# Performance work log

Measured on AMD Instinct MI355X. Metric: run time of the kernel, lower is better.

The kernel has to match this reference:

```python
import jax, jax.numpy as jnp
import numpy as np

N, E, FN, FE, H, B = 8192, 32768, 32, 16, 73, 64
T_MP, T_S2S = 3, 12


def setup_inputs() -> dict:
    key = jax.random.key(0)
    k = jax.random.split(key, 24)
    s = 0.1
    p = lambda i, shape: jax.random.normal(k[i], shape, jnp.float32) * s
    return {
        "node_feats": jax.random.normal(k[0], (N, FN), jnp.float32),
        "edge_feats": jax.random.normal(k[1], (E, FE), jnp.float32),
        "W_in": p(2, (FN, H)), "b_in": p(3, (H,)),
        "ee_W1": p(4, (FE, H)), "ee_b1": p(5, (H,)),
        "ee_W2": p(6, (H, H * H)), "ee_b2": p(7, (H * H,)),
        "gru_Wih": p(8, (3 * H, H)), "gru_Whh": p(9, (3 * H, H)),
        "gru_bih": p(10, (3 * H,)), "gru_bhh": p(11, (3 * H,)),
        "lstm_Wih": p(12, (4 * H, 2 * H)), "lstm_Whh": p(13, (4 * H, H)),
        "lstm_bih": p(14, (4 * H,)), "lstm_bhh": p(15, (4 * H,)),
        "W_out": p(16, (H, 1)), "b_out": p(17, (1,)),
        "Esrc": jax.random.randint(k[18], (E,), 0, N),
        "Etgt": jax.random.randint(k[19], (E,), 0, N),
        "batch": jnp.sort(jax.random.randint(k[20], (N,), 0, B)),
    }


def reference(node_feats, edge_feats, W_in, b_in, ee_W1, ee_b1, ee_W2, ee_b2,
              gru_Wih, gru_Whh, gru_bih, gru_bhh,
              lstm_Wih, lstm_Whh, lstm_bih, lstm_bhh, W_out, b_out,
              Esrc, Etgt, batch):
    # EdgeEncoderMLP: edge features -> per-edge HxH weight matrices (Gilmer edge network)
    A = (jax.nn.relu(edge_feats @ ee_W1 + ee_b1) @ ee_W2 + ee_b2).reshape(E, H, H)
    h = node_feats @ W_in + b_in  # [N, H]

    def mp_step(h, _):
        m = jnp.einsum('eij,ej->ei', A, h[Esrc])           # per-edge matvec (gather-matmul)
        agg = jax.ops.segment_sum(m, Etgt, num_segments=N)  # scatter-add to targets
        # GRUCell update (torch gate order r,z,n)
        gi = agg @ gru_Wih.T + gru_bih
        gh = h @ gru_Whh.T + gru_bhh
        ir, iz, inn = jnp.split(gi, 3, axis=-1)
        hr, hz, hn = jnp.split(gh, 3, axis=-1)
        r = jax.nn.sigmoid(ir + hr)
        z = jax.nn.sigmoid(iz + hz)
        n = jnp.tanh(inn + r * hn)
        return (1.0 - z) * n + z * h, None

    h, _ = jax.lax.scan(mp_step, h, None, length=T_MP)

    # Set2Set pooling with a 1-layer LSTM (torch gate order i,f,g,o)
    def s2s_step(carry, _):
        q_star, hh, cc = carry
        gates = q_star @ lstm_Wih.T + lstm_bih + hh @ lstm_Whh.T + lstm_bhh
        i, f, g, o = jnp.split(gates, 4, axis=-1)
        cc = jax.nn.sigmoid(f) * cc + jax.nn.sigmoid(i) * jnp.tanh(g)
        hh = jax.nn.sigmoid(o) * jnp.tanh(cc)
        q = hh                                              # [B, H]
        e = jnp.sum(h * q[batch], axis=-1)                  # [N] attention logits
        emax = jax.ops.segment_max(e, batch, num_segments=B)
        a = jnp.exp(e - emax[batch])
        a = a / jax.ops.segment_sum(a, batch, num_segments=B)[batch]
        r = jax.ops.segment_sum(a[:, None] * h, batch, num_segments=B)
        return (jnp.concatenate([q, r], axis=-1), hh, cc), None

    init = (jnp.zeros((B, 2 * H), h.dtype), jnp.zeros((B, H), h.dtype),
            jnp.zeros((B, H), h.dtype))
    (q_star, _, _), _ = jax.lax.scan(s2s_step, init, None, length=T_S2S)
    return q_star[:, :H] @ W_out + b_out  # [B, 1]
```

## Files before the change

### kernel.cpp

```cpp
#include <hip/hip_runtime.h>

typedef _Float16 f16;
typedef f16 f16x2 __attribute__((ext_vector_type(2)));
typedef f16 f16x4 __attribute__((ext_vector_type(4)));
typedef f16 f16x8 __attribute__((ext_vector_type(8)));
typedef float f32x4 __attribute__((ext_vector_type(4)));

#define AS1 __attribute__((address_space(1)))
#define AS3 __attribute__((address_space(3)))

#define NN 8192
#define EE 32768

#if __has_builtin(__builtin_amdgcn_fdot2)
#define HAS_FDOT2 1
#else
#define HAS_FDOT2 0
#endif

__device__ __forceinline__ void glds16(const void* g, void* l) {
  __builtin_amdgcn_global_load_lds((const AS1 unsigned int*)g, (AS3 unsigned int*)l, 16, 0, 0);
}
__device__ __forceinline__ void stage_bytes(const void* g, void* s, int nbytes, int tid) {
  const int lane = tid & 63;
  for (int off = tid * 16; off < nbytes; off += 4096)
    glds16((const char*)g + off, (char*)s + (off - lane * 16));
}

__global__ void prep_kernel(
    const float* __restrict__ nf, const float* __restrict__ ef,
    const float* __restrict__ W_in, const float* __restrict__ b_in,
    const float* __restrict__ W1, const float* __restrict__ b1,
    const float* __restrict__ W2, const float* __restrict__ b2,
    const float* __restrict__ gWih, const float* __restrict__ gWhh,
    const float* __restrict__ lWih, const float* __restrict__ lWhh,
    const int* __restrict__ batch, const int* __restrict__ Etgt,
    float* __restrict__ h, f16* __restrict__ hf, f16* __restrict__ ehh,
    f16* __restrict__ W2f, f16* __restrict__ WihT, f16* __restrict__ WhhT,
    f16* __restrict__ Wcat, int* __restrict__ segstarts,
    int* __restrict__ count, int* __restrict__ bucket) {
  int t = blockIdx.x * 256 + threadIdx.x;
  if (t < 786432) {
    int n = t / 96, i = t - n * 96;
    float v = 0.f;
    if (i < 73) {
      v = b_in[i];
      const float* nr = nf + n * 32;
      #pragma unroll
      for (int f = 0; f < 32; ++f) v += nr[f] * W_in[f * 73 + i];
    }
    h[t] = v; hf[t] = (f16)v;
    return;
  }
  t -= 786432;
  if (t < 2621440) {
    int e = t / 80, k = t - e * 80;
    float v;
    if (k < 73) {
      v = b1[k];
      const float* er = ef + e * 16;
      #pragma unroll
      for (int f = 0; f < 16; ++f) v += er[f] * W1[f * 73 + k];
      v = fmaxf(v, 0.f);
    } else v = (k == 73) ? 1.f : 0.f;
    ehh[t] = (f16)v;
    return;
  }
  t -= 2621440;
  if (t < 614400) {
    int kg = t / 7680, r = t - kg * 7680;
    int nt = r / 1536, r2 = r - nt * 1536;
    int ks = r2 / 512, r3 = r2 - ks * 512;
    int l = r3 >> 3, j = r3 & 7;
    int mr = l & 15, q = l >> 4;
    int i = nt * 16 + mr, jj = ks * 32 + q * 8 + j;
    float v = 0.f;
    if (i < 73 && jj < 73) {
      if (kg < 73) v = W2[kg * 5329 + i * 73 + jj];
      else if (kg == 73) v = b2[i * 73 + jj];
    }
    W2f[t] = (f16)v;
    return;
  }
  t -= 614400;
  if (t < 43008) {
    int half = t / 21504, r = t - half * 21504;
    int g = r / 96, k = r - g * 96;
    float v = 0.f;
    if (g < 219 && k < 73) v = half ? gWhh[g * 73 + k] : gWih[g * 73 + k];
    (half ? WhhT : WihT)[r] = (f16)v;
    return;
  }
  t -= 43008;
  if (t < 67744) {
    int g = t / 232, k = t - g * 232;
    float v = 0.f;
    if (k < 73) v = lWih[g * 146 + k] + lWhh[g * 73 + k];
    else if (k >= 76 && k < 149) v = lWih[g * 146 + (k - 3)];
    Wcat[t] = (f16)v;
    return;
  }
  t -= 67744;
  if (t < 65) {
    int key = t, lo = 0, hi = NN;
    while (lo < hi) { int mid = (lo + hi) >> 1; if (batch[mid] < key) lo = mid + 1; else hi = mid; }
    segstarts[t] = lo;
    return;
  }
  t -= 65;
  if (t < EE) {
    int tg = Etgt[t];
    int slot = atomicAdd(&count[tg], 1);
    if (slot < 64) bucket[tg * 64 + slot] = t;
  }
}

__global__ __launch_bounds__(256, 2) void vgemm_kernel(
    const f16* __restrict__ ehh, const f16* __restrict__ hf,
    const f16* __restrict__ W2f, const int* __restrict__ Esrc,
    f16* __restrict__ m) {
  __shared__ __align__(16) f16 w2s[2][15360];
  const int tid = threadIdx.x;
  const int bm = blockIdx.x & 127, ksp = blockIdx.x >> 7;
  const int e0 = bm * 256;
  const int kg0 = ksp * 20;
  const int wave = tid >> 6, lane = tid & 63;
  const int q = lane >> 4, mr = lane & 15;

  stage_bytes(W2f + kg0 * 7680, w2s[0], 30720, tid);

  f16x8 hsv[4][3];
  size_t er80[4];
  #pragma unroll
  for (int mt = 0; mt < 4; ++mt) {
    int er = e0 + wave * 64 + mt * 16 + mr;
    int srcn = Esrc[er];
    er80[mt] = (size_t)er * 80;
    #pragma unroll
    for (int ks = 0; ks < 3; ++ks)
      hsv[mt][ks] = *(const f16x8*)(hf + (size_t)srcn * 96 + ks * 32 + q * 8);
  }

  f32x4 zero = {0.f, 0.f, 0.f, 0.f};
  f32x4 acc[4][5];
  #pragma unroll
  for (int mt = 0; mt < 4; ++mt)
    #pragma unroll
    for (int nt = 0; nt < 5; ++nt) acc[mt][nt] = zero;

  for (int ch = 0; ch < 10; ++ch) {
    f16x2 evq[4];
    #pragma unroll
    for (int mt = 0; mt < 4; ++mt)
      evq[mt] = *(const f16x2*)(ehh + er80[mt] + kg0 + ch * 2);
    __syncthreads();
    if (ch + 1 < 10)
      stage_bytes(W2f + (kg0 + (ch + 1) * 2) * 7680, w2s[(ch + 1) & 1], 30720, tid);
    const f16* wb = w2s[ch & 1];
    #pragma unroll
    for (int i = 0; i < 2; ++i) {
      f16x8 af[4][3];
      #pragma unroll
      for (int mt = 0; mt < 4; ++mt) {
        f16 ev = evq[mt][i];
        f16x8 evv = {ev, ev, ev, ev, ev, ev, ev, ev};
        #pragma unroll
        for (int ks = 0; ks < 3; ++ks) af[mt][ks] = hsv[mt][ks] * evv;
      }
      const f16* wbi = wb + i * 7680;
      #pragma unroll
      for (int nt = 0; nt < 5; ++nt) {
        #pragma unroll
        for (int ks = 0; ks < 3; ++ks) {
          f16x8 bf = *(const f16x8*)(wbi + (nt * 3 + ks) * 512 + lane * 8);
          #pragma unroll
          for (int mt = 0; mt < 4; ++mt)
            acc[mt][nt] = __builtin_amdgcn_mfma_f32_16x16x32_f16(af[mt][ks], bf, acc[mt][nt], 0, 0, 0);
        }
      }
    }
  }
  #pragma unroll
  for (int mt = 0; mt < 4; ++mt) {
    #pragma unroll
    for (int reg = 0; reg < 4; ++reg) {
      int er = e0 + wave * 64 + mt * 16 + q * 4 + reg;
      f16* mp = m + (size_t)er * 320 + ksp * 80;
      #pragma unroll
      for (int nt = 0; nt < 5; ++nt)
        mp[nt * 16 + mr] = (f16)acc[mt][nt][reg];
    }
  }
}

__global__ __launch_bounds__(256, 2) void aggru_kernel(
    const f16* __restrict__ m, const int* __restrict__ count,
    const int* __restrict__ bucket, const f16* __restrict__ WihT,
    const f16* __restrict__ WhhT, const float* __restrict__ bih,
    const float* __restrict__ bhh, float* __restrict__ h, f16* __restrict__ hf) {
  __shared__ __align__(16) f16 Hs[32 * 96];
  __shared__ __align__(16) f16 As[32 * 96];
  __shared__ __align__(16) f16 Gs[2][32][224];
  const int tid = threadIdx.x;
  const int n0 = blockIdx.x * 32;

  stage_bytes(hf + (size_t)n0 * 96, Hs, 6144, tid);
  {
    int n = tid >> 3, j = tid & 7;
    f16x2 z = {(f16)0.f, (f16)0.f};
    *(f16x2*)(As + n * 96 + 80 + j * 2) = z;
  }
  #pragma unroll
  for (int k = 0; k < 10; ++k) {
    int o = tid + k * 256;
    int n = o / 80, i = o - n * 80;
    int cnt = count[n0 + n]; if (cnt > 64) cnt = 64;
    const int* bk = bucket + (size_t)(n0 + n) * 64;
    float s = 0.f;
    for (int j = 0; j < cnt; ++j) {
      const f16* mp = m + (size_t)bk[j] * 320;
      s += ((float)mp[i] + (float)mp[80 + i]) + ((float)mp[160 + i] + (float)mp[240 + i]);
    }
    As[n * 96 + i] = (f16)s;
  }
  __syncthreads();
  const int w = tid >> 6, lane = tid & 63, q = lane >> 4, mr = lane & 15;
  const int g = w & 1, mt = w >> 1;
  const f16* Asrc = g ? Hs : As;
  const f16* B = g ? WhhT : WihT;
  f16x8 af[3];
  #pragma unroll
  for (int ks = 0; ks < 3; ++ks)
    af[ks] = *(const f16x8*)(Asrc + (mt * 16 + mr) * 96 + ks * 32 + q * 8);
  #pragma unroll
  for (int nt = 0; nt < 14; ++nt) {
    f32x4 acc = {0.f, 0.f, 0.f, 0.f};
    #pragma unroll
    for (int ks = 0; ks < 3; ++ks) {
      f16x8 bf = *(const f16x8*)(B + (nt * 16 + mr) * 96 + ks * 32 + q * 8);
      acc = __builtin_amdgcn_mfma_f32_16x16x32_f16(af[ks], bf, acc, 0, 0, 0);
    }
    #pragma unroll
    for (int reg = 0; reg < 4; ++reg)
      Gs[g][mt * 16 + q * 4 + reg][nt * 16 + mr] = (f16)acc[reg];
  }
  __syncthreads();
  #pragma unroll
  for (int k = 0; k < 10; ++k) {
    int idx = tid + k * 256;
    if (idx < 2336) {
      int n = idx / 73, i = idx - n * 73;
      float rr = (float)Gs[0][n][i] + bih[i] + (float)Gs[1][n][i] + bhh[i];
      rr = 1.f / (1.f + __expf(-rr));
      float zz = (float)Gs[0][n][73 + i] + bih[73 + i] + (float)Gs[1][n][73 + i] + bhh[73 + i];
      zz = 1.f / (1.f + __expf(-zz));
      float nx = (float)Gs[0][n][146 + i] + bih[146 + i] + rr * ((float)Gs[1][n][146 + i] + bhh[146 + i]);
      float nn_ = 2.f / (1.f + __expf(-2.f * nx)) - 1.f;
      size_t hi_ = (size_t)(n0 + n) * 96 + i;
      float hv = h[hi_];
      float hn = (1.f - zz) * nn_ + zz * hv;
      h[hi_] = hn;
      hf[hi_] = (f16)hn;
    }
  }
}

__device__ __forceinline__ float wred_sum(float v) {
  #pragma unroll
  for (int off = 32; off; off >>= 1) v += __shfl_xor(v, off, 64);
  return v;
}
__device__ __forceinline__ float dot8(f16x8 w, f16x8 x, float acc) {
#if HAS_FDOT2
  acc = __builtin_amdgcn_fdot2((f16x2)__builtin_shufflevector(w, w, 0, 1),
                               (f16x2)__builtin_shufflevector(x, x, 0, 1), acc, false);
  acc = __builtin_amdgcn_fdot2((f16x2)__builtin_shufflevector(w, w, 2, 3),
                               (f16x2)__builtin_shufflevector(x, x, 2, 3), acc, false);
  acc = __builtin_amdgcn_fdot2((f16x2)__builtin_shufflevector(w, w, 4, 5),
                               (f16x2)__builtin_shufflevector(x, x, 4, 5), acc, false);
  acc = __builtin_amdgcn_fdot2((f16x2)__builtin_shufflevector(w, w, 6, 7),
                               (f16x2)__builtin_shufflevector(x, x, 6, 7), acc, false);
#else
  #pragma unroll
  for (int e = 0; e < 8; ++e) acc += (float)w[e] * (float)x[e];
#endif
  return acc;
}
__device__ __forceinline__ float dot4(f16x4 w, f16x4 x, float acc) {
#if HAS_FDOT2
  acc = __builtin_amdgcn_fdot2((f16x2)__builtin_shufflevector(w, w, 0, 1),
                               (f16x2)__builtin_shufflevector(x, x, 0, 1), acc, false);
  acc = __builtin_amdgcn_fdot2((f16x2)__builtin_shufflevector(w, w, 2, 3),
                               (f16x2)__builtin_shufflevector(x, x, 2, 3), acc, false);
#else
  #pragma unroll
  for (int e = 0; e < 4; ++e) acc += (float)w[e] * (float)x[e];
#endif
  return acc;
}

#define S2SCAP 256
#define NCAP 190

__global__ __launch_bounds__(512, 2) void s2s_kernel(
    const float* __restrict__ h, const f16* __restrict__ hf,
    const f16* __restrict__ Wcat,
    const float* __restrict__ lbih, const float* __restrict__ lbhh,
    const float* __restrict__ Wout, const float* __restrict__ bout,
    const int* __restrict__ segstarts, float* __restrict__ out) {
  __shared__ __align__(16) f16 hseg[NCAP * 84];
  __shared__ __align__(16) f16 xcat[240];
  __shared__ float hhv[80];
  __shared__ float gatesv[292];
  __shared__ float earr[S2SCAP];
  __shared__ float red[4];
  __shared__ __align__(16) float rpart[19 * 80];
  const int t = threadIdx.x, b = blockIdx.x;
  const int wid = t >> 6, lane = t & 63;

  const int s0 = segstarts[b];
  int segT = segstarts[b + 1] - s0;
  if (segT > S2SCAP) segT = S2SCAP;
  const int c = segT < NCAP ? segT : NCAP;

  if (t < 240) xcat[t] = (f16)0.f;
  if (t < 80) hhv[t] = 0.f;
  if (t < S2SCAP) earr[t] = 0.f;

  for (int r = wid; r < NCAP; r += 8) {
    if (lane < 21) {
      f16x4 v = {(f16)0.f, (f16)0.f, (f16)0.f, (f16)0.f};
      if (r < c && lane < 19)
        v = *(const f16x4*)(hf + (size_t)(s0 + r) * 96 + lane * 4);
      *(f16x4*)(hseg + r * 84 + lane * 4) = v;
    }
  }

  const bool isg = (t >= 220);
  const int g2 = t - 220;
  float bias = 0.f;
  if (isg) bias = lbih[g2] + lbhh[g2];
  f16x8 wihF[19];
  {
    const f16* wr = Wcat + (size_t)(isg ? g2 : 0) * 232;
    #pragma unroll
    for (int v = 0; v < 19; ++v) wihF[v] = *(const f16x8*)(wr + v * 8);
  }
  const int nc = t / 10, fo = t - nc * 10;
  float creg = 0.f;
  __syncthreads();

  for (int iter = 0; iter < 12; ++iter) {
    if (isg) {
      float a0 = bias, a1 = 0.f, a2 = 0.f, a3 = 0.f;
      #pragma unroll
      for (int v = 0; v < 19; ++v) {
        f16x8 x = *(const f16x8*)(xcat + v * 8);
        int sel = v & 3;
        if (sel == 0) a0 = dot8(wihF[v], x, a0);
        else if (sel == 1) a1 = dot8(wihF[v], x, a1);
        else if (sel == 2) a2 = dot8(wihF[v], x, a2);
        else a3 = dot8(wihF[v], x, a3);
      }
      gatesv[g2] = (a0 + a1) + (a2 + a3);
    }
    __syncthreads();
    if (t < 73) {
      float ig = 1.f / (1.f + __expf(-gatesv[t]));
      float fg = 1.f / (1.f + __expf(-gatesv[73 + t]));
      float gx = gatesv[146 + t];
      float gg = 2.f / (1.f + __expf(-2.f * gx)) - 1.f;
      float og = 1.f / (1.f + __expf(-gatesv[219 + t]));
      creg = fg * creg + ig * gg;
      float cth = 2.f / (1.f + __expf(-2.f * creg)) - 1.f;
      float hh = og * cth;
      hhv[t] = hh;
      xcat[t] = (f16)hh;
    }
    __syncthreads();
    if (wid < 3) {
      float a = 0.f;
      if (t < c) {
        const f16* hp = hseg + t * 84;
        float e0 = 0.f, e1 = 0.f;
        #pragma unroll
        for (int k = 0; k < 9; ++k) {
          f16x4 h0 = *(const f16x4*)(hp + 8 * k);
          f16x4 h1 = *(const f16x4*)(hp + 8 * k + 4);
          f16x4 x0 = *(const f16x4*)(xcat + 8 * k);
          f16x4 x1 = *(const f16x4*)(xcat + 8 * k + 4);
          e0 = dot4(h0, x0, e0);
          e1 = dot4(h1, x1, e1);
        }
        f16x4 ht = *(const f16x4*)(hp + 72);
        f16x4 xt = *(const f16x4*)(xcat + 72);
        e0 = dot4(ht, xt, e0);
        a = __expf(fminf(e0 + e1, 80.f));
        earr[t] = a;
      }
      float ws = wred_sum(a);
      if (lane == 0) red[wid] = ws;
    }
    if (wid == 0) {
      float fa = 0.f;
      int n = NCAP + lane;
      if (n < segT) {
        const float* hr = h + (size_t)(s0 + n) * 96;
        float e = 0.f;
        for (int i = 0; i < 73; ++i) e += hr[i] * hhv[i];
        fa = __expf(fminf(e, 80.f));
        earr[n] = fa;
      }
      float ws2 = wred_sum(fa);
      if (lane == 0) red[3] = ws2;
    }
    __syncthreads();
    if (t < 190) {
      float r0 = 0.f, r1 = 0.f, r2 = 0.f, r3 = 0.f, r4 = 0.f, r5 = 0.f, r6 = 0.f, r7 = 0.f;
      #pragma unroll
      for (int j = 0; j < 10; ++j) {
        int n = nc * 10 + j;
        float a = earr[n];
        const f16* hp = hseg + n * 84 + fo * 8;
        f16x4 v0 = *(const f16x4*)(hp);
        f16x4 v1 = *(const f16x4*)(hp + 4);
        r0 += a * (float)v0[0]; r1 += a * (float)v0[1];
        r2 += a * (float)v0[2]; r3 += a * (float)v0[3];
        r4 += a * (float)v1[0]; r5 += a * (float)v1[1];
        r6 += a * (float)v1[2]; r7 += a * (float)v1[3];
      }
      if (nc == 18) {
        for (int n = NCAP; n < segT; ++n) {
          float a = earr[n];
          const f16* hp = hf + (size_t)(s0 + n) * 96 + fo * 8;
          f16x4 v0 = *(const f16x4*)(hp);
          f16x4 v1 = *(const f16x4*)(hp + 4);
          r0 += a * (float)v0[0]; r1 += a * (float)v0[1];
          r2 += a * (float)v0[2]; r3 += a * (float)v0[3];
          r4 += a * (float)v1[0]; r5 += a * (float)v1[1];
          r6 += a * (float)v1[2]; r7 += a * (float)v1[3];
        }
      }
      f32x4 wa = {r0, r1, r2, r3}, wb = {r4, r5, r6, r7};
      *(f32x4*)(rpart + nc * 80 + fo * 8) = wa;
      *(f32x4*)(rpart + nc * 80 + fo * 8 + 4) = wb;
    }
    __syncthreads();
    if (t < 80) {
      float S = red[0] + red[1] + red[2] + red[3];
      float invS = (S > 0.f) ? (1.f / S) : 0.f;
      float r = 0.f;
      #pragma unroll
      for (int ch = 0; ch < 19; ++ch) r += rpart[ch * 80 + t];
      if (t < 73) xcat[76 + t] = (f16)(r * invS);
    }
    __syncthreads();
  }
  if (t < 80) gatesv[t] = (t < 73) ? hhv[t] * Wout[t] : 0.f;
  __syncthreads();
  if (t == 0) {
    float a = bout[0];
    for (int i = 0; i < 73; ++i) a += gatesv[i];
    out[b] = a;
  }
}

#define OFF_H      0u
#define OFF_HF     17825792u
#define OFF_EHH    20971520u
#define OFF_W2F    26214400u
#define OFF_WIHT   27443200u
#define OFF_WHHT   27486208u
#define OFF_WCAT   27529216u
#define OFF_SEG    27664704u
#define OFF_CNT    27665024u
#define OFF_BKT    27697792u
#define OFF_M      29794944u

extern "C" void kernel_launch(void* const* d_in, const int* in_sizes, int n_in,
                              void* d_out, int out_size, void* d_ws, size_t ws_size,
                              hipStream_t stream) {
  const float* nf   = (const float*)d_in[0];
  const float* ef   = (const float*)d_in[1];
  const float* W_in = (const float*)d_in[2];
  const float* b_in = (const float*)d_in[3];
  const float* W1   = (const float*)d_in[4];
  const float* b1   = (const float*)d_in[5];
  const float* W2   = (const float*)d_in[6];
  const float* b2   = (const float*)d_in[7];
  const float* gWih = (const float*)d_in[8];
  const float* gWhh = (const float*)d_in[9];
  const float* gbih = (const float*)d_in[10];
  const float* gbhh = (const float*)d_in[11];
  const float* lWih = (const float*)d_in[12];
  const float* lWhh = (const float*)d_in[13];
  const float* lbih = (const float*)d_in[14];
  const float* lbhh = (const float*)d_in[15];
  const float* Wout = (const float*)d_in[16];
  const float* bout = (const float*)d_in[17];
  const int* Esrc   = (const int*)d_in[18];
  const int* Etgt   = (const int*)d_in[19];
  const int* batch  = (const int*)d_in[20];

  char* ws = (char*)d_ws;
  float* h    = (float*)(ws + OFF_H);
  f16* hf     = (f16*)(ws + OFF_HF);
  f16* ehh    = (f16*)(ws + OFF_EHH);
  f16* W2f    = (f16*)(ws + OFF_W2F);
  f16* WihT   = (f16*)(ws + OFF_WIHT);
  f16* WhhT   = (f16*)(ws + OFF_WHHT);
  f16* Wcat   = (f16*)(ws + OFF_WCAT);
  int* segst  = (int*)(ws + OFF_SEG);
  int* cnt    = (int*)(ws + OFF_CNT);
  int* bkt    = (int*)(ws + OFF_BKT);
  f16* m      = (f16*)(ws + OFF_M);

  hipMemsetAsync(cnt, 0, NN * sizeof(int), stream);
  prep_kernel<<<16273, 256, 0, stream>>>(nf, ef, W_in, b_in, W1, b1, W2, b2,
                                         gWih, gWhh, lWih, lWhh, batch, Etgt,
                                         h, hf, ehh, W2f, WihT, WhhT, Wcat,
                                         segst, cnt, bkt);
  for (int step = 0; step < 3; ++step) {
    vgemm_kernel<<<512, 256, 0, stream>>>(ehh, hf, W2f, Esrc, m);
    aggru_kernel<<<256, 256, 0, stream>>>(m, cnt, bkt, WihT, WhhT, gbih, gbhh, h, hf);
  }
  s2s_kernel<<<64, 512, 0, stream>>>(h, hf, Wcat, lbih, lbhh, Wout, bout, segst,
                                     (float*)d_out);
}
```

Baseline: 374.4 us.

## Shrink vgemm edge tile and split aggregation into standalone gather kernel

The edge GEMM now uses 128-edge blocks, stages one k-slice of W2 per chunk, and raises the occupancy hint, doubling the grid to 1024 blocks. The fused aggregate+GRU kernel is split into a wide gather kernel (2048 blocks) that writes the summed messages to a new f16 buffer, followed by a GRU kernel that handles 64 nodes per block. The goal is more parallelism for the latency-bound gather and better occupancy in vgemm. In exchange it adds an extra launch and a global round trip per step, and the GRU kernel now runs only 128 blocks at one block per CU.

New measurement: 345.4 us. 1.08x faster.

```diff
diff --git a/kernel.cpp b/kernel.cpp
--- a/kernel.cpp
+++ b/kernel.cpp
@@ -115,25 +115,25 @@
   }
 }
 
-__global__ __launch_bounds__(256, 2) void vgemm_kernel(
+__global__ __launch_bounds__(256, 4) void vgemm_kernel(
     const f16* __restrict__ ehh, const f16* __restrict__ hf,
     const f16* __restrict__ W2f, const int* __restrict__ Esrc,
     f16* __restrict__ m) {
-  __shared__ __align__(16) f16 w2s[2][15360];
+  __shared__ __align__(16) f16 w2s[2][7680];
   const int tid = threadIdx.x;
-  const int bm = blockIdx.x & 127, ksp = blockIdx.x >> 7;
-  const int e0 = bm * 256;
+  const int bm = blockIdx.x & 255, ksp = blockIdx.x >> 8;
+  const int e0 = bm * 128;
   const int kg0 = ksp * 20;
   const int wave = tid >> 6, lane = tid & 63;
   const int q = lane >> 4, mr = lane & 15;
 
-  stage_bytes(W2f + kg0 * 7680, w2s[0], 30720, tid);
-
-  f16x8 hsv[4][3];
-  size_t er80[4];
-  #pragma unroll
-  for (int mt = 0; mt < 4; ++mt) {
-    int er = e0 + wave * 64 + mt * 16 + mr;
+  stage_bytes(W2f + kg0 * 7680, w2s[0], 15360, tid);
+
+  f16x8 hsv[2][3];
+  size_t er80[2];
+  #pragma unroll
+  for (int mt = 0; mt < 2; ++mt) {
+    int er = e0 + wave * 32 + mt * 16 + mr;
     int srcn = Esrc[er];
     er80[mt] = (size_t)er * 80;
     #pragma unroll
@@ -142,49 +142,42 @@
   }
 
   f32x4 zero = {0.f, 0.f, 0.f, 0.f};
-  f32x4 acc[4][5];
-  #pragma unroll
-  for (int mt = 0; mt < 4; ++mt)
+  f32x4 acc[2][5];
+  #pragma unroll
+  for (int mt = 0; mt < 2; ++mt)
     #pragma unroll
     for (int nt = 0; nt < 5; ++nt) acc[mt][nt] = zero;
 
-  for (int ch = 0; ch < 10; ++ch) {
-    f16x2 evq[4];
-    #pragma unroll
-    for (int mt = 0; mt < 4; ++mt)
-      evq[mt] = *(const f16x2*)(ehh + er80[mt] + kg0 + ch * 2);
+  for (int ch = 0; ch < 20; ++ch) {
+    f16 ev0 = ehh[er80[0] + kg0 + ch];
+    f16 ev1 = ehh[er80[1] + kg0 + ch];
     __syncthreads();
-    if (ch + 1 < 10)
-      stage_bytes(W2f + (kg0 + (ch + 1) * 2) * 7680, w2s[(ch + 1) & 1], 30720, tid);
+    if (ch + 1 < 20)
+      stage_bytes(W2f + (kg0 + ch + 1) * 7680, w2s[(ch + 1) & 1], 15360, tid);
     const f16* wb = w2s[ch & 1];
-    #pragma unroll
-    for (int i = 0; i < 2; ++i) {
-      f16x8 af[4][3];
-      #pragma unroll
-      for (int mt = 0; mt < 4; ++mt) {
-        f16 ev = evq[mt][i];
-        f16x8 evv = {ev, ev, ev, ev, ev, ev, ev, ev};
-        #pragma unroll
-        for (int ks = 0; ks < 3; ++ks) af[mt][ks] = hsv[mt][ks] * evv;
+    f16x8 af[2][3];
+    f16x8 ev0v = {ev0, ev0, ev0, ev0, ev0, ev0, ev0, ev0};
+    f16x8 ev1v = {ev1, ev1, ev1, ev1, ev1, ev1, ev1, ev1};
+    #pragma unroll
+    for (int ks = 0; ks < 3; ++ks) {
+      af[0][ks] = hsv[0][ks] * ev0v;
+      af[1][ks] = hsv[1][ks] * ev1v;
+    }
+    #pragma unroll
+    for (int nt = 0; nt < 5; ++nt) {
+      #pragma unroll
+      for (int ks = 0; ks < 3; ++ks) {
+        f16x8 bf = *(const f16x8*)(wb + (nt * 3 + ks) * 512 + lane * 8);
+        acc[0][nt] = __builtin_amdgcn_mfma_f32_16x16x32_f16(af[0][ks], bf, acc[0][nt], 0, 0, 0);
+        acc[1][nt] = __builtin_amdgcn_mfma_f32_16x16x32_f16(af[1][ks], bf, acc[1][nt], 0, 0, 0);
       }
-      const f16* wbi = wb + i * 7680;
-      #pragma unroll
-      for (int nt = 0; nt < 5; ++nt) {
-        #pragma unroll
-        for (int ks = 0; ks < 3; ++ks) {
-          f16x8 bf = *(const f16x8*)(wbi + (nt * 3 + ks) * 512 + lane * 8);
-          #pragma unroll
-          for (int mt = 0; mt < 4; ++mt)
-            acc[mt][nt] = __builtin_amdgcn_mfma_f32_16x16x32_f16(af[mt][ks], bf, acc[mt][nt], 0, 0, 0);
-        }
-      }
-    }
-  }
-  #pragma unroll
-  for (int mt = 0; mt < 4; ++mt) {
+    }
+  }
+  #pragma unroll
+  for (int mt = 0; mt < 2; ++mt) {
     #pragma unroll
     for (int reg = 0; reg < 4; ++reg) {
-      int er = e0 + wave * 64 + mt * 16 + q * 4 + reg;
+      int er = e0 + wave * 32 + mt * 16 + q * 4 + reg;
       f16* mp = m + (size_t)er * 320 + ksp * 80;
       #pragma unroll
       for (int nt = 0; nt < 5; ++nt)
@@ -193,75 +186,76 @@
   }
 }
 
-__global__ __launch_bounds__(256, 2) void aggru_kernel(
-    const f16* __restrict__ m, const int* __restrict__ count,
-    const int* __restrict__ bucket, const f16* __restrict__ WihT,
-    const f16* __restrict__ WhhT, const float* __restrict__ bih,
-    const float* __restrict__ bhh, float* __restrict__ h, f16* __restrict__ hf) {
-  __shared__ __align__(16) f16 Hs[32 * 96];
-  __shared__ __align__(16) f16 As[32 * 96];
-  __shared__ __align__(16) f16 Gs[2][32][224];
-  const int tid = threadIdx.x;
-  const int n0 = blockIdx.x * 32;
-
-  stage_bytes(hf + (size_t)n0 * 96, Hs, 6144, tid);
-  {
-    int n = tid >> 3, j = tid & 7;
-    f16x2 z = {(f16)0.f, (f16)0.f};
-    *(f16x2*)(As + n * 96 + 80 + j * 2) = z;
-  }
-  #pragma unroll
-  for (int k = 0; k < 10; ++k) {
-    int o = tid + k * 256;
-    int n = o / 80, i = o - n * 80;
-    int cnt = count[n0 + n]; if (cnt > 64) cnt = 64;
-    const int* bk = bucket + (size_t)(n0 + n) * 64;
-    float s = 0.f;
+__global__ void gather_kernel(const f16* __restrict__ m, const int* __restrict__ count,
+                              const int* __restrict__ bucket, f16* __restrict__ aggf) {
+  int t = blockIdx.x * 384 + threadIdx.x;
+  int n = t / 96, i = t - n * 96;
+  float s = 0.f;
+  if (i < 80) {
+    int cnt = count[n]; if (cnt > 64) cnt = 64;
+    const int* bk = bucket + n * 64;
     for (int j = 0; j < cnt; ++j) {
       const f16* mp = m + (size_t)bk[j] * 320;
       s += ((float)mp[i] + (float)mp[80 + i]) + ((float)mp[160 + i] + (float)mp[240 + i]);
     }
-    As[n * 96 + i] = (f16)s;
-  }
-  __syncthreads();
+  }
+  aggf[t] = (f16)s;
+}
+
+__global__ __launch_bounds__(256, 1) void grufuse_kernel(
+    const f16* __restrict__ aggf, const f16* __restrict__ hf,
+    const f16* __restrict__ WihT, const f16* __restrict__ WhhT,
+    const float* __restrict__ bih, const float* __restrict__ bhh,
+    float* __restrict__ h, f16* __restrict__ hfout) {
+  __shared__ __align__(16) f16 As[64 * 96];
+  __shared__ __align__(16) f16 Hs[64 * 96];
+  __shared__ __align__(16) f16 Gs[2][64][224];
+  const int tid = threadIdx.x;
+  const int n0 = blockIdx.x * 64;
+  stage_bytes(aggf + (size_t)n0 * 96, As, 12288, tid);
+  stage_bytes(hf + (size_t)n0 * 96, Hs, 12288, tid);
   const int w = tid >> 6, lane = tid & 63, q = lane >> 4, mr = lane & 15;
-  const int g = w & 1, mt = w >> 1;
+  const int g = w >> 1, sub = w & 1;
   const f16* Asrc = g ? Hs : As;
   const f16* B = g ? WhhT : WihT;
-  f16x8 af[3];
-  #pragma unroll
-  for (int ks = 0; ks < 3; ++ks)
-    af[ks] = *(const f16x8*)(Asrc + (mt * 16 + mr) * 96 + ks * 32 + q * 8);
+  __syncthreads();
+  f16x8 af[2][3];
+  #pragma unroll
+  for (int mt = 0; mt < 2; ++mt)
+    #pragma unroll
+    for (int ks = 0; ks < 3; ++ks)
+      af[mt][ks] = *(const f16x8*)(Asrc + (sub * 32 + mt * 16 + mr) * 96 + ks * 32 + q * 8);
   #pragma unroll
   for (int nt = 0; nt < 14; ++nt) {
-    f32x4 acc = {0.f, 0.f, 0.f, 0.f};
+    f32x4 acc[2];
+    acc[0] = (f32x4){0.f, 0.f, 0.f, 0.f};
+    acc[1] = (f32x4){0.f, 0.f, 0.f, 0.f};
     #pragma unroll
     for (int ks = 0; ks < 3; ++ks) {
       f16x8 bf = *(const f16x8*)(B + (nt * 16 + mr) * 96 + ks * 32 + q * 8);
-      acc = __builtin_amdgcn_mfma_f32_16x16x32_f16(af[ks], bf, acc, 0, 0, 0);
-    }
-    #pragma unroll
-    for (int reg = 0; reg < 4; ++reg)
-      Gs[g][mt * 16 + q * 4 + reg][nt * 16 + mr] = (f16)acc[reg];
+      acc[0] = __builtin_amdgcn_mfma_f32_16x16x32_f16(af[0][ks], bf, acc[0], 0, 0, 0);
+      acc[1] = __builtin_amdgcn_mfma_f32_16x16x32_f16(af[1][ks], bf, acc[1], 0, 0, 0);
+    }
+    #pragma unroll
+    for (int mt = 0; mt < 2; ++mt)
+      #pragma unroll
+      for (int reg = 0; reg < 4; ++reg)
+        Gs[g][sub * 32 + mt * 16 + q * 4 + reg][nt * 16 + mr] = (f16)acc[mt][reg];
   }
   __syncthreads();
-  #pragma unroll
-  for (int k = 0; k < 10; ++k) {
-    int idx = tid + k * 256;
-    if (idx < 2336) {
-      int n = idx / 73, i = idx - n * 73;
-      float rr = (float)Gs[0][n][i] + bih[i] + (float)Gs[1][n][i] + bhh[i];
-      rr = 1.f / (1.f + __expf(-rr));
-      float zz = (float)Gs[0][n][73 + i] + bih[73 + i] + (float)Gs[1][n][73 + i] + bhh[73 + i];
-      zz = 1.f / (1.f + __expf(-zz));
-      float nx = (float)Gs[0][n][146 + i] + bih[146 + i] + rr * ((float)Gs[1][n][146 + i] + bhh[146 + i]);
-      float nn_ = 2.f / (1.f + __expf(-2.f * nx)) - 1.f;
-      size_t hi_ = (size_t)(n0 + n) * 96 + i;
-      float hv = h[hi_];
-      float hn = (1.f - zz) * nn_ + zz * hv;
-      h[hi_] = hn;
-      hf[hi_] = (f16)hn;
-    }
+  for (int idx = tid; idx < 4672; idx += 256) {
+    int n = idx / 73, i = idx - n * 73;
+    float rr = (float)Gs[0][n][i] + bih[i] + (float)Gs[1][n][i] + bhh[i];
+    rr = 1.f / (1.f + __expf(-rr));
+    float zz = (float)Gs[0][n][73 + i] + bih[73 + i] + (float)Gs[1][n][73 + i] + bhh[73 + i];
+    zz = 1.f / (1.f + __expf(-zz));
+    float nx = (float)Gs[0][n][146 + i] + bih[146 + i] + rr * ((float)Gs[1][n][146 + i] + bhh[146 + i]);
+    float nn_ = 2.f / (1.f + __expf(-2.f * nx)) - 1.f;
+    size_t hi_ = (size_t)(n0 + n) * 96 + i;
+    float hv = h[hi_];
+    float hn = (1.f - zz) * nn_ + zz * hv;
+    h[hi_] = hn;
+    hfout[hi_] = (f16)hn;
   }
 }
 
@@ -467,6 +461,7 @@
 
 #define OFF_H      0u
 #define OFF_HF     17825792u
+#define OFF_AGGF   19398656u
 #define OFF_EHH    20971520u
 #define OFF_W2F    26214400u
 #define OFF_WIHT   27443200u
@@ -505,6 +500,7 @@
   char* ws = (char*)d_ws;
   float* h    = (float*)(ws + OFF_H);
   f16* hf     = (f16*)(ws + OFF_HF);
+  f16* aggf   = (f16*)(ws + OFF_AGGF);
   f16* ehh    = (f16*)(ws + OFF_EHH);
   f16* W2f    = (f16*)(ws + OFF_W2F);
   f16* WihT   = (f16*)(ws + OFF_WIHT);
@@ -521,8 +517,9 @@
                                          h, hf, ehh, W2f, WihT, WhhT, Wcat,
                                          segst, cnt, bkt);
   for (int step = 0; step < 3; ++step) {
-    vgemm_kernel<<<512, 256, 0, stream>>>(ehh, hf, W2f, Esrc, m);
-    aggru_kernel<<<256, 256, 0, stream>>>(m, cnt, bkt, WihT, WhhT, gbih, gbhh, h, hf);
+    vgemm_kernel<<<1024, 256, 0, stream>>>(ehh, hf, W2f, Esrc, m);
+    gather_kernel<<<2048, 384, 0, stream>>>(m, cnt, bkt, aggf);
+    grufuse_kernel<<<128, 256, 0, stream>>>(aggf, hf, WihT, WhhT, gbih, gbhh, h, hf);
   }
   s2s_kernel<<<64, 512, 0, stream>>>(h, hf, Wcat, lbih, lbhh, Wout, bout, segst,
                                      (float*)d_out);
```
